# Kernel tuning notes

Measured on AMD Instinct MI355X. Metric: run time of the kernel, lower is better.

The kernel has to match this reference:

```python
import jax, jax.numpy as jnp
import numpy as np

B, T = 16384, 128  # batch, n_frames


def setup_inputs() -> dict:
    key = jax.random.key(0)
    k0, k1, k2, k3, k4, k5 = jax.random.split(key, 6)
    dir = jax.random.normal(k0, (B, 3), dtype=jnp.float32)
    R = jax.random.normal(k1, (B, T, 3, 3), dtype=jnp.float32)
    s = 1.0 / np.sqrt(3.0)  # torch LSTM default init scale (uniform +-1/sqrt(hidden))
    W_ih = jax.random.uniform(k2, (12, 3), jnp.float32, -s, s)
    W_hh = jax.random.uniform(k3, (12, 3), jnp.float32, -s, s)
    b_ih = jax.random.uniform(k4, (12,), jnp.float32, -s, s)
    b_hh = jax.random.uniform(k5, (12,), jnp.float32, -s, s)
    return {"dir": dir, "R": R, "W_ih": W_ih, "W_hh": W_hh, "b_ih": b_ih, "b_hh": b_hh}


def _rot_step(v, Rm):
    # v: [B,3], Rm: [B,3,3] -> Rm @ v
    nv = jnp.einsum('bij,bj->bi', Rm, v)
    return nv, nv


def _build_dirs(dir, R):
    n_frames = R.shape[1]
    half = n_frames // 2
    # Backward chain: dirs[i] = R[half-1-i]^T @ ... @ R[half-1]^T @ dir
    Rt_back = jnp.swapaxes(jnp.flip(R[:, :half], axis=1), 2, 3)  # [B, half, 3, 3]
    _, back = jax.lax.scan(_rot_step, dir, jnp.swapaxes(Rt_back, 0, 1))  # [half, B, 3]
    # Forward chain: dirs[i] = R[i-1] @ ... @ R[half] @ dir for i in half+1..n-1
    Rf = jnp.swapaxes(R[:, half:n_frames - 1], 0, 1)  # [n-1-half, B, 3, 3]
    _, fwd = jax.lax.scan(_rot_step, dir, Rf)  # [n-1-half, B, 3]
    dirs_tm = jnp.concatenate([back, dir[None], fwd], axis=0)  # time-major [T, B, 3]
    return dirs_tm, half


def _lstm(dirs_tm, W_ih, W_hh, b_ih, b_hh):
    Bsz = dirs_tm.shape[1]
    h0 = jnp.zeros((Bsz, 3), dirs_tm.dtype)
    c0 = jnp.zeros((Bsz, 3), dirs_tm.dtype)
    bias = b_ih + b_hh

    def step(carry, x):
        h, c = carry
        gates = x @ W_ih.T + h @ W_hh.T + bias  # [B,12]
        i = jax.nn.sigmoid(gates[:, 0:3])
        f = jax.nn.sigmoid(gates[:, 3:6])
        g = jnp.tanh(gates[:, 6:9])
        o = jax.nn.sigmoid(gates[:, 9:12])
        c = f * c + i * g
        h = o * jnp.tanh(c)
        return (h, c), h

    _, h_seq = jax.lax.scan(step, (h0, c0), dirs_tm)  # [T, B, 3]
    return h_seq


def reference(dir, R, W_ih, W_hh, b_ih, b_hh):
    dirs_tm, half = _build_dirs(dir, R)
    h_seq = _lstm(dirs_tm, W_ih, W_hh, b_ih, b_hh)
    dirs_out = jnp.swapaxes(dirs_tm, 0, 1)  # [B, T, 3]
    return dirs_out.at[:, half, :].set(h_seq[half])
```

## Files before the change

kernel.cpp:

```cpp
#include <hip/hip_runtime.h>

typedef float f4 __attribute__((ext_vector_type(4)));
typedef float f4u __attribute__((ext_vector_type(4), aligned(4)));

struct M3 { float m[3][3]; };

#define ELEM(q, n) ((q)[(n) >> 2][(n) & 3])

__device__ __forceinline__ M3 matmul(const M3& A, const M3& B) {
  M3 C;
#pragma unroll
  for (int i = 0; i < 3; ++i)
#pragma unroll
    for (int j = 0; j < 3; ++j)
      C.m[i][j] = A.m[i][0]*B.m[0][j] + A.m[i][1]*B.m[1][j] + A.m[i][2]*B.m[2][j];
  return C;
}

__device__ __forceinline__ M3 mk(const f4 (&q)[9], int k) {
  M3 A;
#pragma unroll
  for (int i = 0; i < 3; ++i)
#pragma unroll
    for (int j = 0; j < 3; ++j)
      A.m[i][j] = ELEM(q, 9*k + 3*i + j);
  return A;
}

template <int CTRL>
__device__ __forceinline__ float dppf(float v) {
  return __int_as_float(
      __builtin_amdgcn_mov_dpp(__float_as_int(v), CTRL, 0xf, 0xf, true));
}

template <int D>
__device__ __forceinline__ M3 dpp_shr_mat(const M3& A) {
  M3 C;
#pragma unroll
  for (int i = 0; i < 3; ++i)
#pragma unroll
    for (int j = 0; j < 3; ++j)
      C.m[i][j] = dppf<0x110 + D>(A.m[i][j]);
  return C;
}

__device__ __forceinline__ float sigm(float z) {
  return __builtin_amdgcn_rcpf(1.0f + __expf(-z));
}
__device__ __forceinline__ float tanh_(float z) {
  float e = __expf(2.0f * z);
  return 1.0f - 2.0f * __builtin_amdgcn_rcpf(e + 1.0f);
}

template <int CTRL>
__device__ __forceinline__ float quad_bcast(float v) {
  return __int_as_float(
      __builtin_amdgcn_mov_dpp(__float_as_int(v), CTRL, 0xf, 0xf, true));
}

__global__ __launch_bounds__(256, 4) void fused_kernel(
    const float* __restrict__ dir, const float* __restrict__ R,
    const float* __restrict__ Wih, const float* __restrict__ Whh,
    const float* __restrict__ bih, const float* __restrict__ bhh,
    float* __restrict__ out, int B, int nbBack) {
  __shared__ f4 xrows[64 * 33];

  const int tid = threadIdx.x;
  const int e = tid >> 3;
  const int s = tid & 7;

  if ((int)blockIdx.x < nbBack) {
    const int b = blockIdx.x * 32 + e;
    const bool valid = (b < B);
    const int bc = valid ? b : 0;
    const float* Rb = R + (size_t)bc * 1152;
    const int lo = 56 - 8 * s;

    f4 qa[9], qb[9];
    {
      const f4* pA = (const f4*)(Rb + lo * 9);
      const f4* pB = (const f4*)(Rb + (lo + 4) * 9);
#pragma unroll
      for (int i = 0; i < 9; ++i) { qa[i] = pA[i]; qb[i] = pB[i]; }
    }
    const float d0 = dir[3*bc+0], d1 = dir[3*bc+1], d2 = dir[3*bc+2];

    M3 P = mk(qa, 0);
#pragma unroll
    for (int k = 1; k < 4; ++k) P = matmul(mk(qa, k), P);
#pragma unroll
    for (int k = 0; k < 4; ++k) P = matmul(mk(qb, k), P);

    M3 I = P;
    {
      M3 Sh = dpp_shr_mat<1>(I); M3 T = matmul(Sh, I);
#pragma unroll
      for (int i = 0; i < 3; ++i)
#pragma unroll
        for (int j = 0; j < 3; ++j) I.m[i][j] = (s >= 1) ? T.m[i][j] : I.m[i][j];
    }
    {
      M3 Sh = dpp_shr_mat<2>(I); M3 T = matmul(Sh, I);
#pragma unroll
      for (int i = 0; i < 3; ++i)
#pragma unroll
        for (int j = 0; j < 3; ++j) I.m[i][j] = (s >= 2) ? T.m[i][j] : I.m[i][j];
    }
    {
      M3 Sh = dpp_shr_mat<4>(I); M3 T = matmul(Sh, I);
#pragma unroll
      for (int i = 0; i < 3; ++i)
#pragma unroll
        for (int j = 0; j < 3; ++j) I.m[i][j] = (s >= 4) ? T.m[i][j] : I.m[i][j];
    }

    float w0 = I.m[0][0]*d0 + I.m[1][0]*d1 + I.m[2][0]*d2;
    float w1 = I.m[0][1]*d0 + I.m[1][1]*d1 + I.m[2][1]*d2;
    float w2 = I.m[0][2]*d0 + I.m[1][2]*d1 + I.m[2][2]*d2;
    float p0 = dppf<0x111>(w0), p1 = dppf<0x111>(w1), p2 = dppf<0x111>(w2);
    float v0 = (s == 0) ? d0 : p0;
    float v1 = (s == 0) ? d1 : p1;
    float v2 = (s == 0) ? d2 : p2;

    float row[24];
#pragma unroll
    for (int j = 0; j < 8; ++j) {
      M3 A = (j < 4) ? mk(qb, 3 - j) : mk(qa, 7 - j);
      float n0 = v0*A.m[0][0] + v1*A.m[1][0] + v2*A.m[2][0];
      float n1 = v0*A.m[0][1] + v1*A.m[1][1] + v2*A.m[2][1];
      float n2 = v0*A.m[0][2] + v1*A.m[1][2] + v2*A.m[2][2];
      v0 = n0; v1 = n1; v2 = n2;
      row[3*j+0] = n0; row[3*j+1] = n1; row[3*j+2] = n2;
    }

    if (valid) {
      float* ob = out + (size_t)b * 384 + 24 * s;
#pragma unroll
      for (int kk = 0; kk < 6; ++kk) {
        f4 vv = { row[4*kk+0], row[4*kk+1], row[4*kk+2], row[4*kk+3] };
        ((f4u*)ob)[kk] = vv;
      }
    }
#pragma unroll
    for (int j = 0; j < 8; ++j) {
      f4 vv = { row[3*j+0], row[3*j+1], row[3*j+2], 0.f };
      xrows[(8*s + j) * 33 + e] = vv;
    }

    __syncthreads();

    const int wv = tid >> 6, ln = tid & 63;
    if (ln >= 32) return;
    const int e2 = wv * 8 + (ln >> 2);
    const int u = ln & 3, uu = (u == 3) ? 0 : u;
    const int b2 = blockIdx.x * 32 + e2;
    if (b2 >= B) return;

    const float wii0 = Wih[uu*3+0],     wii1 = Wih[uu*3+1],     wii2 = Wih[uu*3+2];
    const float wif0 = Wih[(3+uu)*3+0], wif1 = Wih[(3+uu)*3+1], wif2 = Wih[(3+uu)*3+2];
    const float wig0 = Wih[(6+uu)*3+0], wig1 = Wih[(6+uu)*3+1], wig2 = Wih[(6+uu)*3+2];
    const float wio0 = Wih[(9+uu)*3+0], wio1 = Wih[(9+uu)*3+1], wio2 = Wih[(9+uu)*3+2];
    const float whi0 = Whh[uu*3+0],     whi1 = Whh[uu*3+1],     whi2 = Whh[uu*3+2];
    const float whf0 = Whh[(3+uu)*3+0], whf1 = Whh[(3+uu)*3+1], whf2 = Whh[(3+uu)*3+2];
    const float whg0 = Whh[(6+uu)*3+0], whg1 = Whh[(6+uu)*3+1], whg2 = Whh[(6+uu)*3+2];
    const float who0 = Whh[(9+uu)*3+0], who1 = Whh[(9+uu)*3+1], who2 = Whh[(9+uu)*3+2];
    const float bsi = bih[uu]   + bhh[uu];
    const float bsf = bih[3+uu] + bhh[3+uu];
    const float bsg = bih[6+uu] + bhh[6+uu];
    const float bso = bih[9+uu] + bhh[9+uu];
    const float dd0 = dir[3*b2+0], dd1 = dir[3*b2+1], dd2 = dir[3*b2+2];

    float h0 = 0.f, h1 = 0.f, h2 = 0.f, cc = 0.f, hl = 0.f;

#define LSTEP(x0_, x1_, x2_)                                                  \
  {                                                                           \
    float zi = bsi + wii0*(x0_) + wii1*(x1_) + wii2*(x2_)                     \
                   + whi0*h0 + whi1*h1 + whi2*h2;                             \
    float zf = bsf + wif0*(x0_) + wif1*(x1_) + wif2*(x2_)                     \
                   + whf0*h0 + whf1*h1 + whf2*h2;                             \
    float zg = bsg + wig0*(x0_) + wig1*(x1_) + wig2*(x2_)                     \
                   + whg0*h0 + whg1*h1 + whg2*h2;                             \
    float zo = bso + wio0*(x0_) + wio1*(x1_) + wio2*(x2_)                     \
                   + who0*h0 + who1*h1 + who2*h2;                             \
    float ai = sigm(zi), af = sigm(zf), ag = tanh_(zg), ao = sigm(zo);        \
    cc = af*cc + ai*ag;                                                       \
    float hn = ao * tanh_(cc);                                                \
    hl = hn;                                                                  \
    h0 = quad_bcast<0x00>(hn);                                                \
    h1 = quad_bcast<0x55>(hn);                                                \
    h2 = quad_bcast<0xAA>(hn);                                                \
  }

    f4 xa[8], xb[8];
#pragma unroll
    for (int j = 0; j < 8; ++j) xa[j] = xrows[j * 33 + e2];
#pragma unroll
    for (int c = 0; c < 8; ++c) {
      if (c < 7) {
        if ((c & 1) == 0) {
#pragma unroll
          for (int j = 0; j < 8; ++j) xb[j] = xrows[((c+1)*8 + j) * 33 + e2];
        } else {
#pragma unroll
          for (int j = 0; j < 8; ++j) xa[j] = xrows[((c+1)*8 + j) * 33 + e2];
        }
      }
#pragma unroll
      for (int j = 0; j < 8; ++j) {
        f4 x = ((c & 1) == 0) ? xa[j] : xb[j];
        LSTEP(x[0], x[1], x[2]);
      }
    }
    LSTEP(dd0, dd1, dd2);
#undef LSTEP

    if (u < 3) out[(size_t)b2 * 384 + 192 + u] = hl;

  } else {
    const int b = ((int)blockIdx.x - nbBack) * 32 + e;
    const bool valid = (b < B);
    const int bc = valid ? b : 0;
    const float* Rb = R + (size_t)bc * 1152;
    const int lo = 64 + 8 * s;

    f4 qa[9], qb[9];
    {
      const f4* pA = (const f4*)(Rb + lo * 9);
      const f4* pB = (const f4*)(Rb + (lo + 4) * 9);
#pragma unroll
      for (int i = 0; i < 9; ++i) { qa[i] = pA[i]; qb[i] = pB[i]; }
    }
    const float d0 = dir[3*bc+0], d1 = dir[3*bc+1], d2 = dir[3*bc+2];

    M3 P = mk(qa, 0);
#pragma unroll
    for (int k = 1; k < 4; ++k) P = matmul(mk(qa, k), P);
#pragma unroll
    for (int k = 0; k < 4; ++k) P = matmul(mk(qb, k), P);

    M3 I = P;
    {
      M3 Sh = dpp_shr_mat<1>(I); M3 T = matmul(I, Sh);
#pragma unroll
      for (int i = 0; i < 3; ++i)
#pragma unroll
        for (int j = 0; j < 3; ++j) I.m[i][j] = (s >= 1) ? T.m[i][j] : I.m[i][j];
    }
    {
      M3 Sh = dpp_shr_mat<2>(I); M3 T = matmul(I, Sh);
#pragma unroll
      for (int i = 0; i < 3; ++i)
#pragma unroll
        for (int j = 0; j < 3; ++j) I.m[i][j] = (s >= 2) ? T.m[i][j] : I.m[i][j];
    }
    {
      M3 Sh = dpp_shr_mat<4>(I); M3 T = matmul(I, Sh);
#pragma unroll
      for (int i = 0; i < 3; ++i)
#pragma unroll
        for (int j = 0; j < 3; ++j) I.m[i][j] = (s >= 4) ? T.m[i][j] : I.m[i][j];
    }

    float w0 = I.m[0][0]*d0 + I.m[0][1]*d1 + I.m[0][2]*d2;
    float w1 = I.m[1][0]*d0 + I.m[1][1]*d1 + I.m[1][2]*d2;
    float w2 = I.m[2][0]*d0 + I.m[2][1]*d1 + I.m[2][2]*d2;
    float p0 = dppf<0x111>(w0), p1 = dppf<0x111>(w1), p2 = dppf<0x111>(w2);
    float v0 = (s == 0) ? d0 : p0;
    float v1 = (s == 0) ? d1 : p1;
    float v2 = (s == 0) ? d2 : p2;

    float row[24];
#pragma unroll
    for (int j = 0; j < 8; ++j) {
      M3 A = (j < 4) ? mk(qa, j) : mk(qb, j - 4);
      float n0 = A.m[0][0]*v0 + A.m[0][1]*v1 + A.m[0][2]*v2;
      float n1 = A.m[1][0]*v0 + A.m[1][1]*v1 + A.m[1][2]*v2;
      float n2 = A.m[2][0]*v0 + A.m[2][1]*v1 + A.m[2][2]*v2;
      v0 = n0; v1 = n1; v2 = n2;
      row[3*j+0] = n0; row[3*j+1] = n1; row[3*j+2] = n2;
    }

    if (valid) {
      float* ob = out + (size_t)b * 384 + (size_t)(65 + 8*s) * 3;
#pragma unroll
      for (int kk = 0; kk < 5; ++kk) {
        f4u vv = { row[4*kk+0], row[4*kk+1], row[4*kk+2], row[4*kk+3] };
        *(f4u*)(ob + 4*kk) = vv;
      }
      ob[20] = row[20];
      if (s < 7) { ob[21] = row[21]; ob[22] = row[22]; ob[23] = row[23]; }
    }
  }
}

extern "C" void kernel_launch(void* const* d_in, const int* in_sizes, int n_in,
                              void* d_out, int out_size, void* d_ws, size_t ws_size,
                              hipStream_t stream) {
  const float* dir = (const float*)d_in[0];
  const float* R   = (const float*)d_in[1];
  const float* Wih = (const float*)d_in[2];
  const float* Whh = (const float*)d_in[3];
  const float* bih = (const float*)d_in[4];
  const float* bhh = (const float*)d_in[5];
  float* out = (float*)d_out;

  const int B = in_sizes[0] / 3;
  const int nbBack = (B + 31) / 32;
  const int grid = nbBack * 2;
  hipLaunchKernelGGL(fused_kernel, dim3(grid), dim3(256), 0, stream,
                     dir, R, Wih, Whh, bih, bhh, out, B, nbBack);
}
```

Before: 35.77 us.

## Use single-wave blocks with coalesced R staging through LDS

Shrinks blocks from 256 threads (32 batch elements) to one 64-thread wavefront (8 batch elements) and quadruples the grid. The R half-slab for the block is loaded with fully coalesced float4 reads into padded LDS, and each lane then reads its 8 matrices from LDS instead of issuing strided per-thread global loads. The __syncthreads is dropped because the block is a single wave. The forward and backward branches share one code path selected by a flag. The change targets global-load coalescing and barrier cost, and adds an LDS round trip and more blocks, with only half of each wave active during the LSTM phase.

```diff
diff --git a/kernel.cpp b/kernel.cpp
--- a/kernel.cpp
+++ b/kernel.cpp
@@ -17,7 +17,7 @@
   return C;
 }
 
-__device__ __forceinline__ M3 mk(const f4 (&q)[9], int k) {
+__device__ __forceinline__ M3 mk18(const f4 (&q)[18], int k) {
   M3 A;
 #pragma unroll
   for (int i = 0; i < 3; ++i)
@@ -58,40 +58,58 @@
       __builtin_amdgcn_mov_dpp(__float_as_int(v), CTRL, 0xf, 0xf, true));
 }
 
-__global__ __launch_bounds__(256, 4) void fused_kernel(
+__global__ __launch_bounds__(64, 2) void fused_kernel(
     const float* __restrict__ dir, const float* __restrict__ R,
     const float* __restrict__ Wih, const float* __restrict__ Whh,
     const float* __restrict__ bih, const float* __restrict__ bhh,
     float* __restrict__ out, int B, int nbBack) {
-  __shared__ f4 xrows[64 * 33];
-
-  const int tid = threadIdx.x;
-  const int e = tid >> 3;
-  const int s = tid & 7;
-
-  if ((int)blockIdx.x < nbBack) {
-    const int b = blockIdx.x * 32 + e;
-    const bool valid = (b < B);
-    const int bc = valid ? b : 0;
-    const float* Rb = R + (size_t)bc * 1152;
-    const int lo = 56 - 8 * s;
-
-    f4 qa[9], qb[9];
-    {
-      const f4* pA = (const f4*)(Rb + lo * 9);
-      const f4* pB = (const f4*)(Rb + (lo + 4) * 9);
-#pragma unroll
-      for (int i = 0; i < 9; ++i) { qa[i] = pA[i]; qb[i] = pB[i]; }
-    }
-    const float d0 = dir[3*bc+0], d1 = dir[3*bc+1], d2 = dir[3*bc+2];
-
-    M3 P = mk(qa, 0);
-#pragma unroll
-    for (int k = 1; k < 4; ++k) P = matmul(mk(qa, k), P);
-#pragma unroll
-    for (int k = 0; k < 4; ++k) P = matmul(mk(qb, k), P);
-
-    M3 I = P;
+  __shared__ __align__(16) f4 lds[8 * 145];
+
+  const int lane = threadIdx.x;
+  const int e = lane >> 3;
+  const int s = lane & 7;
+  const bool isBack = ((int)blockIdx.x < nbBack);
+  const int blk = isBack ? (int)blockIdx.x : ((int)blockIdx.x - nbBack);
+  const int b0 = blk * 8;
+  const int b = b0 + e;
+  const bool valid = (b < B);
+  const int bc = valid ? b : (B - 1);
+  const int halfOff = isBack ? 0 : 576;
+
+  {
+    f4 tb[18];
+#pragma unroll
+    for (int k = 0; k < 18; ++k) {
+      const int c = lane + 64 * k;
+      const int ec = c / 144;
+      const int rc = c - ec * 144;
+      int be = b0 + ec; be = (be < B) ? be : (B - 1);
+      tb[k] = *(const f4*)(R + (size_t)be * 1152 + halfOff + rc * 4);
+    }
+#pragma unroll
+    for (int k = 0; k < 18; ++k) {
+      const int c = lane + 64 * k;
+      const int ec = c / 144;
+      const int rc = c - ec * 144;
+      lds[ec * 145 + rc] = tb[k];
+    }
+  }
+
+  f4 q[18];
+  {
+    const int off = e * 145 + (isBack ? (126 - 18 * s) : (18 * s));
+#pragma unroll
+    for (int i = 0; i < 18; ++i) q[i] = lds[off + i];
+  }
+
+  const float d0 = dir[3*bc+0], d1 = dir[3*bc+1], d2 = dir[3*bc+2];
+
+  M3 P = mk18(q, 0);
+#pragma unroll
+  for (int k = 1; k < 8; ++k) P = matmul(mk18(q, k), P);
+
+  M3 I = P;
+  if (isBack) {
     {
       M3 Sh = dpp_shr_mat<1>(I); M3 T = matmul(Sh, I);
 #pragma unroll
@@ -113,64 +131,119 @@
 #pragma unroll
         for (int j = 0; j < 3; ++j) I.m[i][j] = (s >= 4) ? T.m[i][j] : I.m[i][j];
     }
-
-    float w0 = I.m[0][0]*d0 + I.m[1][0]*d1 + I.m[2][0]*d2;
-    float w1 = I.m[0][1]*d0 + I.m[1][1]*d1 + I.m[2][1]*d2;
-    float w2 = I.m[0][2]*d0 + I.m[1][2]*d1 + I.m[2][2]*d2;
-    float p0 = dppf<0x111>(w0), p1 = dppf<0x111>(w1), p2 = dppf<0x111>(w2);
-    float v0 = (s == 0) ? d0 : p0;
-    float v1 = (s == 0) ? d1 : p1;
-    float v2 = (s == 0) ? d2 : p2;
-
-    float row[24];
+  } else {
+    {
+      M3 Sh = dpp_shr_mat<1>(I); M3 T = matmul(I, Sh);
+#pragma unroll
+      for (int i = 0; i < 3; ++i)
+#pragma unroll
+        for (int j = 0; j < 3; ++j) I.m[i][j] = (s >= 1) ? T.m[i][j] : I.m[i][j];
+    }
+    {
+      M3 Sh = dpp_shr_mat<2>(I); M3 T = matmul(I, Sh);
+#pragma unroll
+      for (int i = 0; i < 3; ++i)
+#pragma unroll
+        for (int j = 0; j < 3; ++j) I.m[i][j] = (s >= 2) ? T.m[i][j] : I.m[i][j];
+    }
+    {
+      M3 Sh = dpp_shr_mat<4>(I); M3 T = matmul(I, Sh);
+#pragma unroll
+      for (int i = 0; i < 3; ++i)
+#pragma unroll
+        for (int j = 0; j < 3; ++j) I.m[i][j] = (s >= 4) ? T.m[i][j] : I.m[i][j];
+    }
+  }
+
+  float w0, w1, w2;
+  if (isBack) {
+    w0 = I.m[0][0]*d0 + I.m[1][0]*d1 + I.m[2][0]*d2;
+    w1 = I.m[0][1]*d0 + I.m[1][1]*d1 + I.m[2][1]*d2;
+    w2 = I.m[0][2]*d0 + I.m[1][2]*d1 + I.m[2][2]*d2;
+  } else {
+    w0 = I.m[0][0]*d0 + I.m[0][1]*d1 + I.m[0][2]*d2;
+    w1 = I.m[1][0]*d0 + I.m[1][1]*d1 + I.m[1][2]*d2;
+    w2 = I.m[2][0]*d0 + I.m[2][1]*d1 + I.m[2][2]*d2;
+  }
+  float p0 = dppf<0x111>(w0), p1 = dppf<0x111>(w1), p2 = dppf<0x111>(w2);
+  float v0 = (s == 0) ? d0 : p0;
+  float v1 = (s == 0) ? d1 : p1;
+  float v2 = (s == 0) ? d2 : p2;
+
+  float row[24];
+  if (isBack) {
 #pragma unroll
     for (int j = 0; j < 8; ++j) {
-      M3 A = (j < 4) ? mk(qb, 3 - j) : mk(qa, 7 - j);
+      M3 A = mk18(q, 7 - j);
       float n0 = v0*A.m[0][0] + v1*A.m[1][0] + v2*A.m[2][0];
       float n1 = v0*A.m[0][1] + v1*A.m[1][1] + v2*A.m[2][1];
       float n2 = v0*A.m[0][2] + v1*A.m[1][2] + v2*A.m[2][2];
       v0 = n0; v1 = n1; v2 = n2;
       row[3*j+0] = n0; row[3*j+1] = n1; row[3*j+2] = n2;
     }
-
+  } else {
+#pragma unroll
+    for (int j = 0; j < 8; ++j) {
+      M3 A = mk18(q, j);
+      float n0 = A.m[0][0]*v0 + A.m[0][1]*v1 + A.m[0][2]*v2;
+      float n1 = A.m[1][0]*v0 + A.m[1][1]*v1 + A.m[1][2]*v2;
+      float n2 = A.m[2][0]*v0 + A.m[2][1]*v1 + A.m[2][2]*v2;
+      v0 = n0; v1 = n1; v2 = n2;
+      row[3*j+0] = n0; row[3*j+1] = n1; row[3*j+2] = n2;
+    }
+  }
+
+  if (!isBack) {
     if (valid) {
-      float* ob = out + (size_t)b * 384 + 24 * s;
-#pragma unroll
-      for (int kk = 0; kk < 6; ++kk) {
-        f4 vv = { row[4*kk+0], row[4*kk+1], row[4*kk+2], row[4*kk+3] };
-        ((f4u*)ob)[kk] = vv;
+      float* ob = out + (size_t)b * 384 + (size_t)(65 + 8*s) * 3;
+#pragma unroll
+      for (int kk = 0; kk < 5; ++kk) {
+        f4u vv = { row[4*kk+0], row[4*kk+1], row[4*kk+2], row[4*kk+3] };
+        *(f4u*)(ob + 4*kk) = vv;
       }
-    }
-#pragma unroll
-    for (int j = 0; j < 8; ++j) {
-      f4 vv = { row[3*j+0], row[3*j+1], row[3*j+2], 0.f };
-      xrows[(8*s + j) * 33 + e] = vv;
-    }
-
-    __syncthreads();
-
-    const int wv = tid >> 6, ln = tid & 63;
-    if (ln >= 32) return;
-    const int e2 = wv * 8 + (ln >> 2);
-    const int u = ln & 3, uu = (u == 3) ? 0 : u;
-    const int b2 = blockIdx.x * 32 + e2;
-    if (b2 >= B) return;
-
-    const float wii0 = Wih[uu*3+0],     wii1 = Wih[uu*3+1],     wii2 = Wih[uu*3+2];
-    const float wif0 = Wih[(3+uu)*3+0], wif1 = Wih[(3+uu)*3+1], wif2 = Wih[(3+uu)*3+2];
-    const float wig0 = Wih[(6+uu)*3+0], wig1 = Wih[(6+uu)*3+1], wig2 = Wih[(6+uu)*3+2];
-    const float wio0 = Wih[(9+uu)*3+0], wio1 = Wih[(9+uu)*3+1], wio2 = Wih[(9+uu)*3+2];
-    const float whi0 = Whh[uu*3+0],     whi1 = Whh[uu*3+1],     whi2 = Whh[uu*3+2];
-    const float whf0 = Whh[(3+uu)*3+0], whf1 = Whh[(3+uu)*3+1], whf2 = Whh[(3+uu)*3+2];
-    const float whg0 = Whh[(6+uu)*3+0], whg1 = Whh[(6+uu)*3+1], whg2 = Whh[(6+uu)*3+2];
-    const float who0 = Whh[(9+uu)*3+0], who1 = Whh[(9+uu)*3+1], who2 = Whh[(9+uu)*3+2];
-    const float bsi = bih[uu]   + bhh[uu];
-    const float bsf = bih[3+uu] + bhh[3+uu];
-    const float bsg = bih[6+uu] + bhh[6+uu];
-    const float bso = bih[9+uu] + bhh[9+uu];
-    const float dd0 = dir[3*b2+0], dd1 = dir[3*b2+1], dd2 = dir[3*b2+2];
-
-    float h0 = 0.f, h1 = 0.f, h2 = 0.f, cc = 0.f, hl = 0.f;
+      ob[20] = row[20];
+      if (s < 7) { ob[21] = row[21]; ob[22] = row[22]; ob[23] = row[23]; }
+    }
+    return;
+  }
+
+  if (valid) {
+    float* ob = out + (size_t)b * 384 + 24 * s;
+#pragma unroll
+    for (int kk = 0; kk < 6; ++kk) {
+      f4 vv = { row[4*kk+0], row[4*kk+1], row[4*kk+2], row[4*kk+3] };
+      ((f4*)ob)[kk] = vv;
+    }
+  }
+
+#pragma unroll
+  for (int j = 0; j < 8; ++j) {
+    f4 vv = { row[3*j+0], row[3*j+1], row[3*j+2], 0.f };
+    lds[(8*s + j) * 9 + e] = vv;
+  }
+
+  if (lane >= 32) return;
+  const int e2 = lane >> 2;
+  const int u = lane & 3, uu = (u == 3) ? 0 : u;
+  const int b2 = b0 + e2;
+  const bool valid2 = (b2 < B);
+  const int b2c = valid2 ? b2 : 0;
+
+  const float wii0 = Wih[uu*3+0],     wii1 = Wih[uu*3+1],     wii2 = Wih[uu*3+2];
+  const float wif0 = Wih[(3+uu)*3+0], wif1 = Wih[(3+uu)*3+1], wif2 = Wih[(3+uu)*3+2];
+  const float wig0 = Wih[(6+uu)*3+0], wig1 = Wih[(6+uu)*3+1], wig2 = Wih[(6+uu)*3+2];
+  const float wio0 = Wih[(9+uu)*3+0], wio1 = Wih[(9+uu)*3+1], wio2 = Wih[(9+uu)*3+2];
+  const float whi0 = Whh[uu*3+0],     whi1 = Whh[uu*3+1],     whi2 = Whh[uu*3+2];
+  const float whf0 = Whh[(3+uu)*3+0], whf1 = Whh[(3+uu)*3+1], whf2 = Whh[(3+uu)*3+2];
+  const float whg0 = Whh[(6+uu)*3+0], whg1 = Whh[(6+uu)*3+1], whg2 = Whh[(6+uu)*3+2];
+  const float who0 = Whh[(9+uu)*3+0], who1 = Whh[(9+uu)*3+1], who2 = Whh[(9+uu)*3+2];
+  const float bsi = bih[uu]   + bhh[uu];
+  const float bsf = bih[3+uu] + bhh[3+uu];
+  const float bsg = bih[6+uu] + bhh[6+uu];
+  const float bso = bih[9+uu] + bhh[9+uu];
+  const float dd0 = dir[3*b2c+0], dd1 = dir[3*b2c+1], dd2 = dir[3*b2c+2];
+
+  float h0 = 0.f, h1 = 0.f, h2 = 0.f, cc = 0.f, hl = 0.f;
 
 #define LSTEP(x0_, x1_, x2_)                                                  \
   {                                                                           \
@@ -191,106 +264,30 @@
     h2 = quad_bcast<0xAA>(hn);                                                \
   }
 
-    f4 xa[8], xb[8];
-#pragma unroll
-    for (int j = 0; j < 8; ++j) xa[j] = xrows[j * 33 + e2];
-#pragma unroll
-    for (int c = 0; c < 8; ++c) {
-      if (c < 7) {
-        if ((c & 1) == 0) {
-#pragma unroll
-          for (int j = 0; j < 8; ++j) xb[j] = xrows[((c+1)*8 + j) * 33 + e2];
-        } else {
-#pragma unroll
-          for (int j = 0; j < 8; ++j) xa[j] = xrows[((c+1)*8 + j) * 33 + e2];
-        }
+  f4 xa[8], xb[8];
+#pragma unroll
+  for (int j = 0; j < 8; ++j) xa[j] = lds[j * 9 + e2];
+#pragma unroll
+  for (int c = 0; c < 8; ++c) {
+    if (c < 7) {
+      if ((c & 1) == 0) {
+#pragma unroll
+        for (int j = 0; j < 8; ++j) xb[j] = lds[((c+1)*8 + j) * 9 + e2];
+      } else {
+#pragma unroll
+        for (int j = 0; j < 8; ++j) xa[j] = lds[((c+1)*8 + j) * 9 + e2];
       }
-#pragma unroll
-      for (int j = 0; j < 8; ++j) {
-        f4 x = ((c & 1) == 0) ? xa[j] : xb[j];
-        LSTEP(x[0], x[1], x[2]);
-      }
-    }
-    LSTEP(dd0, dd1, dd2);
+    }
+#pragma unroll
+    for (int j = 0; j < 8; ++j) {
+      f4 x = ((c & 1) == 0) ? xa[j] : xb[j];
+      LSTEP(x[0], x[1], x[2]);
+    }
+  }
+  LSTEP(dd0, dd1, dd2);
 #undef LSTEP
 
-    if (u < 3) out[(size_t)b2 * 384 + 192 + u] = hl;
-
-  } else {
-    const int b = ((int)blockIdx.x - nbBack) * 32 + e;
-    const bool valid = (b < B);
-    const int bc = valid ? b : 0;
-    const float* Rb = R + (size_t)bc * 1152;
-    const int lo = 64 + 8 * s;
-
-    f4 qa[9], qb[9];
-    {
-      const f4* pA = (const f4*)(Rb + lo * 9);
-      const f4* pB = (const f4*)(Rb + (lo + 4) * 9);
-#pragma unroll
-      for (int i = 0; i < 9; ++i) { qa[i] = pA[i]; qb[i] = pB[i]; }
-    }
-    const float d0 = dir[3*bc+0], d1 = dir[3*bc+1], d2 = dir[3*bc+2];
-
-    M3 P = mk(qa, 0);
-#pragma unroll
-    for (int k = 1; k < 4; ++k) P = matmul(mk(qa, k), P);
-#pragma unroll
-    for (int k = 0; k < 4; ++k) P = matmul(mk(qb, k), P);
-
-    M3 I = P;
-    {
-      M3 Sh = dpp_shr_mat<1>(I); M3 T = matmul(I, Sh);
-#pragma unroll
-      for (int i = 0; i < 3; ++i)
-#pragma unroll
-        for (int j = 0; j < 3; ++j) I.m[i][j] = (s >= 1) ? T.m[i][j] : I.m[i][j];
-    }
-    {
-      M3 Sh = dpp_shr_mat<2>(I); M3 T = matmul(I, Sh);
-#pragma unroll
-      for (int i = 0; i < 3; ++i)
-#pragma unroll
-        for (int j = 0; j < 3; ++j) I.m[i][j] = (s >= 2) ? T.m[i][j] : I.m[i][j];
-    }
-    {
-      M3 Sh = dpp_shr_mat<4>(I); M3 T = matmul(I, Sh);
-#pragma unroll
-      for (int i = 0; i < 3; ++i)
-#pragma unroll
-        for (int j = 0; j < 3; ++j) I.m[i][j] = (s >= 4) ? T.m[i][j] : I.m[i][j];
-    }
-
-    float w0 = I.m[0][0]*d0 + I.m[0][1]*d1 + I.m[0][2]*d2;
-    float w1 = I.m[1][0]*d0 + I.m[1][1]*d1 + I.m[1][2]*d2;
-    float w2 = I.m[2][0]*d0 + I.m[2][1]*d1 + I.m[2][2]*d2;
-    float p0 = dppf<0x111>(w0), p1 = dppf<0x111>(w1), p2 = dppf<0x111>(w2);
-    float v0 = (s == 0) ? d0 : p0;
-    float v1 = (s == 0) ? d1 : p1;
-    float v2 = (s == 0) ? d2 : p2;
-
-    float row[24];
-#pragma unroll
-    for (int j = 0; j < 8; ++j) {
-      M3 A = (j < 4) ? mk(qa, j) : mk(qb, j - 4);
-      float n0 = A.m[0][0]*v0 + A.m[0][1]*v1 + A.m[0][2]*v2;
-      float n1 = A.m[1][0]*v0 + A.m[1][1]*v1 + A.m[1][2]*v2;
-      float n2 = A.m[2][0]*v0 + A.m[2][1]*v1 + A.m[2][2]*v2;
-      v0 = n0; v1 = n1; v2 = n2;
-      row[3*j+0] = n0; row[3*j+1] = n1; row[3*j+2] = n2;
-    }
-
-    if (valid) {
-      float* ob = out + (size_t)b * 384 + (size_t)(65 + 8*s) * 3;
-#pragma unroll
-      for (int kk = 0; kk < 5; ++kk) {
-        f4u vv = { row[4*kk+0], row[4*kk+1], row[4*kk+2], row[4*kk+3] };
-        *(f4u*)(ob + 4*kk) = vv;
-      }
-      ob[20] = row[20];
-      if (s < 7) { ob[21] = row[21]; ob[22] = row[22]; ob[23] = row[23]; }
-    }
-  }
+  if (valid2 && u < 3) out[(size_t)b2 * 384 + 192 + u] = hl;
 }
 
 extern "C" void kernel_launch(void* const* d_in, const int* in_sizes, int n_in,
@@ -305,8 +302,8 @@
   float* out = (float*)d_out;
 
   const int B = in_sizes[0] / 3;
-  const int nbBack = (B + 31) / 32;
+  const int nbBack = (B + 7) / 8;
   const int grid = nbBack * 2;
-  hipLaunchKernelGGL(fused_kernel, dim3(grid), dim3(256), 0, stream,
+  hipLaunchKernelGGL(fused_kernel, dim3(grid), dim3(64), 0, stream,
                      dir, R, Wih, Whh, bih, bhh, out, B, nbBack);
 }
```

Measured after the change: 36.45 us. Within noise of the previous version (+1.9%).
